# Optimization experiments

Measured on AMD Instinct MI355X. Metric: run time of the kernel, lower is better.

The kernel has to match this reference:

```python
import jax, jax.numpy as jnp
import numpy as np

B, S, CTXD, QD, ATTD = 32, 4096, 512, 512, 256

def setup_inputs() -> dict:
    key = jax.random.key(0)
    ks = jax.random.split(key, 7)
    qry = jax.random.normal(ks[0], (B, QD), dtype=jnp.float32)
    ctx = jax.random.normal(ks[1], (B, S, CTXD), dtype=jnp.float32)
    ctx_mask = jax.random.randint(ks[2], (B, S), 0, 2, dtype=jnp.int32)
    # ensure no all-zero row (would make softmax NaN)
    ctx_mask = ctx_mask.at[:, 0].set(1)
    sc = 1.0 / np.sqrt(CTXD + QD)
    W = jax.random.uniform(ks[3], (CTXD + QD, ATTD), jnp.float32, -sc, sc)
    b = jax.random.uniform(ks[4], (ATTD,), jnp.float32, -sc, sc)
    sc2 = 1.0 / np.sqrt(ATTD)
    w2 = jax.random.uniform(ks[5], (ATTD, 1), jnp.float32, -sc2, sc2)
    b2 = jax.random.uniform(ks[6], (1,), jnp.float32, -sc2, sc2)
    return {"qry": qry, "ctx": ctx, "ctx_mask": ctx_mask, "W": W, "b": b, "w2": w2, "b2": b2}

def reference(qry, ctx, ctx_mask, W, b, w2, b2):
    # cat([ctx, qry_rep]) @ W == ctx @ W_ctx + qry @ W_qry ; avoids the [B,S,ctxdim+qdim] concat
    W_ctx, W_qry = W[:CTXD], W[CTXD:]
    h = jnp.einsum('bsc,ca->bsa', ctx, W_ctx) + (qry @ W_qry)[:, None, :] + b  # [B,S,ATTD]
    y = jnp.tanh(h)
    scores = jnp.einsum('bsa,a->bs', y, w2[:, 0]) + b2[0]  # [B,S]
    scores = scores + jnp.log(ctx_mask.astype(jnp.float32))
    alphas = jax.nn.softmax(scores, axis=-1)  # [B,S]
    summary = jnp.einsum('bsc,bs->bc', ctx, alphas)  # [B,CTXD]
    return (alphas, summary, scores)
```

## Files before the change

kernel.cpp:

```cpp
#include <hip/hip_runtime.h>
#include <math.h>

#define B_ 32
#define S_ 4096
#define CTXD_ 512
#define QD_ 512
#define ATTD_ 256

#define KT 64
#define RT 64
#define NCH (S_ / RT)

#define MASKED_SCORE (-1e30f)

typedef __attribute__((ext_vector_type(8))) short bf16x8;
typedef __attribute__((ext_vector_type(4))) float f32x4;

__device__ __forceinline__ unsigned short f2bf(float f) {
    unsigned u = __float_as_uint(f);
    u += 0x7fff + ((u >> 16) & 1);
    return (unsigned short)(u >> 16);
}
__device__ __forceinline__ unsigned pk2(float lo, float hi) {
    return (unsigned)f2bf(lo) | ((unsigned)f2bf(hi) << 16);
}

__device__ __forceinline__ float fast_tanh(float x) {
    float xc = fminf(fmaxf(x, -15.f), 15.f);
    float t = __expf(2.f * xc);
    return (t - 1.f) / (t + 1.f);
}

__global__ __launch_bounds__(256) void prep_kernel(
    const float* __restrict__ W, const float* __restrict__ qry,
    const float* __restrict__ bias, unsigned short* __restrict__ Wt,
    float* __restrict__ qh) {
    __shared__ unsigned char lds[64 * 66 * 2];
    const int bid = blockIdx.x;
    const int t = threadIdx.x;
    if (bid < 32) {
        unsigned short(*tile)[66] = (unsigned short(*)[66])lds;
        const int kk = (bid >> 2) * 64;
        const int nn = (bid & 3) * 64;
        #pragma unroll
        for (int i = 0; i < 4; ++i) {
            const int r = i * 16 + (t >> 4);
            float4 v = ((const float4*)(W + (size_t)(kk + r) * ATTD_ + nn))[t & 15];
            unsigned short* tr = &tile[r][(t & 15) * 4];
            tr[0] = f2bf(v.x); tr[1] = f2bf(v.y);
            tr[2] = f2bf(v.z); tr[3] = f2bf(v.w);
        }
        __syncthreads();
        const int l8 = (t & 7) * 8;
        #pragma unroll
        for (int p = 0; p < 2; ++p) {
            const int n = p * 32 + (t >> 3);
            uint4 o;
            o.x = (unsigned)tile[l8 + 0][n] | ((unsigned)tile[l8 + 1][n] << 16);
            o.y = (unsigned)tile[l8 + 2][n] | ((unsigned)tile[l8 + 3][n] << 16);
            o.z = (unsigned)tile[l8 + 4][n] | ((unsigned)tile[l8 + 5][n] << 16);
            o.w = (unsigned)tile[l8 + 6][n] | ((unsigned)tile[l8 + 7][n] << 16);
            *(uint4*)(Wt + (size_t)(nn + n) * CTXD_ + kk + l8) = o;
        }
    } else {
        float* q = (float*)lds;
        const int b = bid - 32;
        for (int i = t; i < QD_; i += 256) q[i] = qry[b * QD_ + i];
        __syncthreads();
        float acc = bias[t];
        const float* Wq = W + (size_t)CTXD_ * ATTD_ + t;
        #pragma unroll 8
        for (int k = 0; k < QD_; ++k) acc += q[k] * Wq[(size_t)k * ATTD_];
        qh[b * ATTD_ + t] = acc;
    }
}

__global__ __launch_bounds__(256, 3) void scores_kernel(
    const float* __restrict__ ctx, const unsigned short* __restrict__ Wt,
    const float* __restrict__ qh, const float* __restrict__ w2,
    const float* __restrict__ b2, const int* __restrict__ mask,
    float* __restrict__ scores, float* __restrict__ mstat,
    float* __restrict__ lstat, float* __restrict__ part) {
    __shared__ unsigned char lds_a[RT * 144];
    __shared__ unsigned char lds_b[ATTD_ * 144];
    const int t = threadIdx.x;
    const int b = blockIdx.y;
    const int ch = blockIdx.x;
    const int s0 = ch * RT;
    const int tx = t & 63;
    const int w = t >> 6;
    const int wm = w & 1;
    const int wn = w >> 1;
    const int frow = tx & 15;
    const int fq = tx >> 4;

    f32x4 c00, c01, c02, c03, c04, c05, c06, c07;
    f32x4 c10, c11, c12, c13, c14, c15, c16, c17;
    c00 = c01 = c02 = c03 = c04 = c05 = c06 = c07 = (f32x4)0.f;
    c10 = c11 = c12 = c13 = c14 = c15 = c16 = c17 = (f32x4)0.f;

    const float* ctxb = ctx + ((size_t)b * S_ + s0) * CTXD_;
    const int arow = t >> 2;
    const int akq = t & 3;
    const int bn = t;

    const unsigned char* aBase = lds_a + (wm * 32 + frow) * 144 + fq * 16;
    const unsigned char* bBase = lds_b + (wn * 128 + frow) * 144 + fq * 16;

    const float* sA = ctxb + (size_t)arow * CTXD_ + akq * 16;
    float4 fa0 = ((const float4*)sA)[0];
    float4 fa1 = ((const float4*)sA)[1];
    float4 fa2 = ((const float4*)sA)[2];
    float4 fa3 = ((const float4*)sA)[3];
    const uint4* sB = (const uint4*)(Wt + (size_t)bn * CTXD_);
    uint4 pb0 = sB[0], pb1 = sB[1], pb2 = sB[2], pb3 = sB[3];
    uint4 pb4 = sB[4], pb5 = sB[5], pb6 = sB[6], pb7 = sB[7];

#define MM1(ni, ks, C0, C1)                                                  \
    {                                                                        \
        bf16x8 bf = *(const bf16x8*)(bBase + (ni) * (16 * 144) + (ks) * 64); \
        C0 = __builtin_amdgcn_mfma_f32_16x16x32_bf16(a0, bf, C0, 0, 0, 0);   \
        C1 = __builtin_amdgcn_mfma_f32_16x16x32_bf16(a1, bf, C1, 0, 0, 0);   \
    }
#define MMK(ks)                                                              \
    {                                                                        \
        bf16x8 a0 = *(const bf16x8*)(aBase + (ks) * 64);                     \
        bf16x8 a1 = *(const bf16x8*)(aBase + 16 * 144 + (ks) * 64);          \
        MM1(0, ks, c00, c10) MM1(1, ks, c01, c11) MM1(2, ks, c02, c12)       \
        MM1(3, ks, c03, c13) MM1(4, ks, c04, c14) MM1(5, ks, c05, c15)       \
        MM1(6, ks, c06, c16) MM1(7, ks, c07, c17)                            \
    }

    #pragma unroll 1
    for (int k0 = 0; k0 < CTXD_; k0 += KT) {
        __syncthreads();
        {
            uint4 p;
            p.x = pk2(fa0.x, fa0.y); p.y = pk2(fa0.z, fa0.w);
            p.z = pk2(fa1.x, fa1.y); p.w = pk2(fa1.z, fa1.w);
            *(uint4*)(lds_a + arow * 144 + akq * 32) = p;
            p.x = pk2(fa2.x, fa2.y); p.y = pk2(fa2.z, fa2.w);
            p.z = pk2(fa3.x, fa3.y); p.w = pk2(fa3.z, fa3.w);
            *(uint4*)(lds_a + arow * 144 + akq * 32 + 16) = p;
            uint4* bw = (uint4*)(lds_b + bn * 144);
            bw[0] = pb0; bw[1] = pb1; bw[2] = pb2; bw[3] = pb3;
            bw[4] = pb4; bw[5] = pb5; bw[6] = pb6; bw[7] = pb7;
        }
        __syncthreads();
        if (k0 + KT < CTXD_) {
            const float* sA2 = ctxb + (size_t)arow * CTXD_ + (k0 + KT) + akq * 16;
            fa0 = ((const float4*)sA2)[0];
            fa1 = ((const float4*)sA2)[1];
            fa2 = ((const float4*)sA2)[2];
            fa3 = ((const float4*)sA2)[3];
            const uint4* sB2 = (const uint4*)(Wt + (size_t)bn * CTXD_ + (k0 + KT));
            pb0 = sB2[0]; pb1 = sB2[1]; pb2 = sB2[2]; pb3 = sB2[3];
            pb4 = sB2[4]; pb5 = sB2[5]; pb6 = sB2[6]; pb7 = sB2[7];
        }
        MMK(0)
        MMK(1)
    }
#undef MMK
#undef MM1

    const float* qhb = qh + b * ATTD_ + wn * 128;
    const float* w2b = w2 + wn * 128;
    float p00 = 0.f, p01 = 0.f, p02 = 0.f, p03 = 0.f;
    float p10 = 0.f, p11 = 0.f, p12 = 0.f, p13 = 0.f;
#define EPI(ni, C0, C1)                                                      \
    {                                                                        \
        float qv = qhb[(ni) * 16 + frow];                                    \
        float wv = w2b[(ni) * 16 + frow];                                    \
        p00 += fast_tanh(C0[0] + qv) * wv;                                   \
        p01 += fast_tanh(C0[1] + qv) * wv;                                   \
        p02 += fast_tanh(C0[2] + qv) * wv;                                   \
        p03 += fast_tanh(C0[3] + qv) * wv;                                   \
        p10 += fast_tanh(C1[0] + qv) * wv;                                   \
        p11 += fast_tanh(C1[1] + qv) * wv;                                   \
        p12 += fast_tanh(C1[2] + qv) * wv;                                   \
        p13 += fast_tanh(C1[3] + qv) * wv;                                   \
    }
    EPI(0, c00, c10) EPI(1, c01, c11) EPI(2, c02, c12) EPI(3, c03, c13)
    EPI(4, c04, c14) EPI(5, c05, c15) EPI(6, c06, c16) EPI(7, c07, c17)
#undef EPI
    #pragma unroll
    for (int off = 1; off <= 8; off <<= 1) {
        p00 += __shfl_xor(p00, off, 64);
        p01 += __shfl_xor(p01, off, 64);
        p02 += __shfl_xor(p02, off, 64);
        p03 += __shfl_xor(p03, off, 64);
        p10 += __shfl_xor(p10, off, 64);
        p11 += __shfl_xor(p11, off, 64);
        p12 += __shfl_xor(p12, off, 64);
        p13 += __shfl_xor(p13, off, 64);
    }
    float* sred = (float*)lds_a;
    __syncthreads();
    if (frow == 0) {
        const int base = wn * 64 + wm * 32 + fq * 4;
        sred[base + 0] = p00; sred[base + 1] = p01;
        sred[base + 2] = p02; sred[base + 3] = p03;
        sred[base + 16 + 0] = p10; sred[base + 16 + 1] = p11;
        sred[base + 16 + 2] = p12; sred[base + 16 + 3] = p13;
    }
    __syncthreads();
    float* wl = (float*)lds_b;
    if (t < 64) {
        const int s = s0 + t;
        float sc = sred[t] + sred[64 + t] + b2[0];
        const bool msk = (mask[b * S_ + s] == 0);
        if (msk) sc = MASKED_SCORE;
        scores[b * S_ + s] = sc;
        float mloc = sc;
        #pragma unroll
        for (int off = 1; off < 64; off <<= 1)
            mloc = fmaxf(mloc, __shfl_xor(mloc, off, 64));
        const float ws = msk ? 0.f : __expf(sc - mloc);
        float lloc = ws;
        #pragma unroll
        for (int off = 1; off < 64; off <<= 1)
            lloc += __shfl_xor(lloc, off, 64);
        if (t == 0) {
            mstat[b * NCH + ch] = mloc;
            lstat[b * NCH + ch] = lloc;
        }
        wl[t] = ws;
    }
    __syncthreads();
    const int col = t & 63;
    const int q = t >> 6;
    float4 alo = make_float4(0.f, 0.f, 0.f, 0.f);
    float4 ahi = make_float4(0.f, 0.f, 0.f, 0.f);
    #pragma unroll 4
    for (int s = q; s < RT; s += 4) {
        const float al = wl[s];
        const float4* row = (const float4*)(ctxb + (size_t)s * CTXD_);
        float4 v0 = row[col];
        float4 v1 = row[col + 64];
        alo.x += v0.x * al; alo.y += v0.y * al;
        alo.z += v0.z * al; alo.w += v0.w * al;
        ahi.x += v1.x * al; ahi.y += v1.y * al;
        ahi.z += v1.z * al; ahi.w += v1.w * al;
    }
    float4* buf = (float4*)(lds_b + 1024);
    buf[q * 128 + col] = alo;
    buf[q * 128 + col + 64] = ahi;
    __syncthreads();
    if (t < 128) {
        float4 a0 = buf[t], a1 = buf[128 + t], a2 = buf[256 + t], a3 = buf[384 + t];
        float4 r;
        r.x = a0.x + a1.x + a2.x + a3.x;
        r.y = a0.y + a1.y + a2.y + a3.y;
        r.z = a0.z + a1.z + a2.z + a3.z;
        r.w = a0.w + a1.w + a2.w + a3.w;
        ((float4*)(part + ((size_t)(b * NCH + ch)) * CTXD_))[t] = r;
    }
}

__global__ __launch_bounds__(256) void combine_kernel(
    const float* __restrict__ mstat, const float* __restrict__ lstat,
    const float* __restrict__ part, const float* __restrict__ scores,
    float* __restrict__ alphas, float* __restrict__ summary) {
    const int b = blockIdx.y, seg = blockIdx.x, t = threadIdx.x;
    __shared__ float e[NCH];
    __shared__ float gstat[2];
    if (t < NCH) {
        const float mi = mstat[b * NCH + t];
        const float li = lstat[b * NCH + t];
        float m = mi;
        #pragma unroll
        for (int off = 1; off < 64; off <<= 1)
            m = fmaxf(m, __shfl_xor(m, off, 64));
        const float ei = __expf(mi - m);
        float l = ei * li;
        #pragma unroll
        for (int off = 1; off < 64; off <<= 1)
            l += __shfl_xor(l, off, 64);
        e[t] = ei;
        if (t == 0) { gstat[0] = m; gstat[1] = 1.0f / l; }
    }
    __syncthreads();
    const float m = gstat[0], il = gstat[1];
    const int c4 = t & 31;
    const int grp = t >> 5;
    float4 acc = make_float4(0.f, 0.f, 0.f, 0.f);
    for (int chv = grp; chv < NCH; chv += 8) {
        const float ei = e[chv];
        float4 v =
            ((const float4*)(part + ((size_t)(b * NCH + chv)) * CTXD_ + seg * 128))[c4];
        acc.x += ei * v.x; acc.y += ei * v.y;
        acc.z += ei * v.z; acc.w += ei * v.w;
    }
    __shared__ float4 buf[8][32];
    buf[grp][c4] = acc;
    __syncthreads();
    if (t < 32) {
        float4 r = make_float4(0.f, 0.f, 0.f, 0.f);
        #pragma unroll
        for (int g = 0; g < 8; ++g) {
            float4 v = buf[g][t];
            r.x += v.x; r.y += v.y; r.z += v.z; r.w += v.w;
        }
        r.x *= il; r.y *= il; r.z *= il; r.w *= il;
        ((float4*)(summary + (size_t)b * CTXD_ + seg * 128))[t] = r;
    }
    const int sbase = seg * 1024;
    #pragma unroll
    for (int i = 0; i < 4; ++i) {
        const int s = sbase + i * 256 + t;
        alphas[b * S_ + s] = __expf(scores[b * S_ + s] - m) * il;
    }
}

extern "C" void kernel_launch(void* const* d_in, const int* in_sizes, int n_in,
                              void* d_out, int out_size, void* d_ws,
                              size_t ws_size, hipStream_t stream) {
    const float* qry = (const float*)d_in[0];
    const float* ctx = (const float*)d_in[1];
    const int* mask = (const int*)d_in[2];
    const float* W = (const float*)d_in[3];
    const float* bias = (const float*)d_in[4];
    const float* w2 = (const float*)d_in[5];
    const float* b2 = (const float*)d_in[6];

    float* out = (float*)d_out;
    float* alphas = out;
    float* summary = out + B_ * S_;
    float* scores = out + B_ * S_ + B_ * CTXD_;

    unsigned short* Wt = (unsigned short*)d_ws;
    float* qh = (float*)((char*)d_ws + (size_t)ATTD_ * CTXD_ * 2);
    float* mstat = qh + B_ * ATTD_;
    float* lstat = mstat + B_ * NCH;
    float* part = lstat + B_ * NCH;

    prep_kernel<<<64, 256, 0, stream>>>(W, qry, bias, Wt, qh);
    scores_kernel<<<dim3(NCH, B_), 256, 0, stream>>>(ctx, Wt, qh, w2, b2, mask,
                                                     scores, mstat, lstat, part);
    combine_kernel<<<dim3(4, B_), 256, 0, stream>>>(mstat, lstat, part, scores,
                                                    alphas, summary);
}
```

Before: 449.1 us.

## Pre-swizzle W into MFMA fragment layout and feed MFMAs directly from global memory

The prep kernel now writes W_ctx in bf16, already arranged in the per-lane MFMA fragment order. The scores kernel drops LDS staging and its per-step barriers: each lane loads its ctx fragment straight from global memory, converts it to bf16 in registers, and loads B fragments from the swizzled buffer, across a fully unrolled K loop. This removes LDS traffic and synchronisation, but leaves no explicit prefetch overlap, raises register pressure (launch bounds drop from 3 to 2), and has each wave re-read W through the cache.

```diff
diff --git a/kernel.cpp b/kernel.cpp
--- a/kernel.cpp
+++ b/kernel.cpp
@@ -7,7 +7,6 @@
 #define QD_ 512
 #define ATTD_ 256
 
-#define KT 64
 #define RT 64
 #define NCH (S_ / RT)
 
@@ -24,6 +23,19 @@
 __device__ __forceinline__ unsigned pk2(float lo, float hi) {
     return (unsigned)f2bf(lo) | ((unsigned)f2bf(hi) << 16);
 }
+__device__ __forceinline__ bf16x8 cvt8(float4 lo, float4 hi) {
+    union { unsigned u[4]; bf16x8 v; } r;
+    r.u[0] = pk2(lo.x, lo.y);
+    r.u[1] = pk2(lo.z, lo.w);
+    r.u[2] = pk2(hi.x, hi.y);
+    r.u[3] = pk2(hi.z, hi.w);
+    return r.v;
+}
+__device__ __forceinline__ bf16x8 ld_bf8(const unsigned short* p) {
+    union { uint4 q; bf16x8 v; } r;
+    r.q = *(const uint4*)p;
+    return r.v;
+}
 
 __device__ __forceinline__ float fast_tanh(float x) {
     float xc = fminf(fmaxf(x, -15.f), 15.f);
@@ -33,38 +45,30 @@
 
 __global__ __launch_bounds__(256) void prep_kernel(
     const float* __restrict__ W, const float* __restrict__ qry,
-    const float* __restrict__ bias, unsigned short* __restrict__ Wt,
+    const float* __restrict__ bias, unsigned short* __restrict__ Wtf,
     float* __restrict__ qh) {
-    __shared__ unsigned char lds[64 * 66 * 2];
+    __shared__ float q[QD_];
     const int bid = blockIdx.x;
     const int t = threadIdx.x;
-    if (bid < 32) {
-        unsigned short(*tile)[66] = (unsigned short(*)[66])lds;
-        const int kk = (bid >> 2) * 64;
-        const int nn = (bid & 3) * 64;
-        #pragma unroll
-        for (int i = 0; i < 4; ++i) {
-            const int r = i * 16 + (t >> 4);
-            float4 v = ((const float4*)(W + (size_t)(kk + r) * ATTD_ + nn))[t & 15];
-            unsigned short* tr = &tile[r][(t & 15) * 4];
-            tr[0] = f2bf(v.x); tr[1] = f2bf(v.y);
-            tr[2] = f2bf(v.z); tr[3] = f2bf(v.w);
-        }
-        __syncthreads();
-        const int l8 = (t & 7) * 8;
-        #pragma unroll
-        for (int p = 0; p < 2; ++p) {
-            const int n = p * 32 + (t >> 3);
+    if (bid < 16) {
+        const int n16 = bid;
+        const int lane = t & 63;
+        const int ksl = t >> 6;
+        const int ncol = n16 * 16 + (lane & 15);
+        #pragma unroll
+        for (int r = 0; r < 4; ++r) {
+            const int ks = ksl + r * 4;
+            const int krow = ks * 32 + (lane >> 4) * 8;
+            const float* src = W + (size_t)krow * ATTD_ + ncol;
             uint4 o;
-            o.x = (unsigned)tile[l8 + 0][n] | ((unsigned)tile[l8 + 1][n] << 16);
-            o.y = (unsigned)tile[l8 + 2][n] | ((unsigned)tile[l8 + 3][n] << 16);
-            o.z = (unsigned)tile[l8 + 4][n] | ((unsigned)tile[l8 + 5][n] << 16);
-            o.w = (unsigned)tile[l8 + 6][n] | ((unsigned)tile[l8 + 7][n] << 16);
-            *(uint4*)(Wt + (size_t)(nn + n) * CTXD_ + kk + l8) = o;
+            o.x = pk2(src[0], src[ATTD_]);
+            o.y = pk2(src[2 * ATTD_], src[3 * ATTD_]);
+            o.z = pk2(src[4 * ATTD_], src[5 * ATTD_]);
+            o.w = pk2(src[6 * ATTD_], src[7 * ATTD_]);
+            *(uint4*)(Wtf + ((size_t)(n16 * 16 + ks) * 64 + lane) * 8) = o;
         }
     } else {
-        float* q = (float*)lds;
-        const int b = bid - 32;
+        const int b = bid - 16;
         for (int i = t; i < QD_; i += 256) q[i] = qry[b * QD_ + i];
         __syncthreads();
         float acc = bias[t];
@@ -75,14 +79,15 @@
     }
 }
 
-__global__ __launch_bounds__(256, 3) void scores_kernel(
-    const float* __restrict__ ctx, const unsigned short* __restrict__ Wt,
+__global__ __launch_bounds__(256, 2) void scores_kernel(
+    const float* __restrict__ ctx, const unsigned short* __restrict__ Wtf,
     const float* __restrict__ qh, const float* __restrict__ w2,
     const float* __restrict__ b2, const int* __restrict__ mask,
     float* __restrict__ scores, float* __restrict__ mstat,
     float* __restrict__ lstat, float* __restrict__ part) {
-    __shared__ unsigned char lds_a[RT * 144];
-    __shared__ unsigned char lds_b[ATTD_ * 144];
+    __shared__ float sred[128];
+    __shared__ float wl[64];
+    __shared__ float4 pbuf[512];
     const int t = threadIdx.x;
     const int b = blockIdx.y;
     const int ch = blockIdx.x;
@@ -100,66 +105,31 @@
     c10 = c11 = c12 = c13 = c14 = c15 = c16 = c17 = (f32x4)0.f;
 
     const float* ctxb = ctx + ((size_t)b * S_ + s0) * CTXD_;
-    const int arow = t >> 2;
-    const int akq = t & 3;
-    const int bn = t;
-
-    const unsigned char* aBase = lds_a + (wm * 32 + frow) * 144 + fq * 16;
-    const unsigned char* bBase = lds_b + (wn * 128 + frow) * 144 + fq * 16;
-
-    const float* sA = ctxb + (size_t)arow * CTXD_ + akq * 16;
-    float4 fa0 = ((const float4*)sA)[0];
-    float4 fa1 = ((const float4*)sA)[1];
-    float4 fa2 = ((const float4*)sA)[2];
-    float4 fa3 = ((const float4*)sA)[3];
-    const uint4* sB = (const uint4*)(Wt + (size_t)bn * CTXD_);
-    uint4 pb0 = sB[0], pb1 = sB[1], pb2 = sB[2], pb3 = sB[3];
-    uint4 pb4 = sB[4], pb5 = sB[5], pb6 = sB[6], pb7 = sB[7];
-
-#define MM1(ni, ks, C0, C1)                                                  \
+    const float* aR0 = ctxb + (size_t)(wm * 32 + frow) * CTXD_ + fq * 8;
+    const float* aR1 = aR0 + (size_t)16 * CTXD_;
+    const unsigned short* bB = Wtf + ((size_t)(wn * 8) * 16 * 64 + tx) * 8;
+
+#define MM1(ni, ks)                                                          \
     {                                                                        \
-        bf16x8 bf = *(const bf16x8*)(bBase + (ni) * (16 * 144) + (ks) * 64); \
-        C0 = __builtin_amdgcn_mfma_f32_16x16x32_bf16(a0, bf, C0, 0, 0, 0);   \
-        C1 = __builtin_amdgcn_mfma_f32_16x16x32_bf16(a1, bf, C1, 0, 0, 0);   \
+        bf16x8 bf = ld_bf8(bB + ((size_t)((ni) * 16 + (ks)) * 64) * 8);      \
+        c0##ni = __builtin_amdgcn_mfma_f32_16x16x32_bf16(a0, bf, c0##ni, 0, 0, 0); \
+        c1##ni = __builtin_amdgcn_mfma_f32_16x16x32_bf16(a1, bf, c1##ni, 0, 0, 0); \
     }
 #define MMK(ks)                                                              \
     {                                                                        \
-        bf16x8 a0 = *(const bf16x8*)(aBase + (ks) * 64);                     \
-        bf16x8 a1 = *(const bf16x8*)(aBase + 16 * 144 + (ks) * 64);          \
-        MM1(0, ks, c00, c10) MM1(1, ks, c01, c11) MM1(2, ks, c02, c12)       \
-        MM1(3, ks, c03, c13) MM1(4, ks, c04, c14) MM1(5, ks, c05, c15)       \
-        MM1(6, ks, c06, c16) MM1(7, ks, c07, c17)                            \
-    }
-
-    #pragma unroll 1
-    for (int k0 = 0; k0 < CTXD_; k0 += KT) {
-        __syncthreads();
-        {
-            uint4 p;
-            p.x = pk2(fa0.x, fa0.y); p.y = pk2(fa0.z, fa0.w);
-            p.z = pk2(fa1.x, fa1.y); p.w = pk2(fa1.z, fa1.w);
-            *(uint4*)(lds_a + arow * 144 + akq * 32) = p;
-            p.x = pk2(fa2.x, fa2.y); p.y = pk2(fa2.z, fa2.w);
-            p.z = pk2(fa3.x, fa3.y); p.w = pk2(fa3.z, fa3.w);
-            *(uint4*)(lds_a + arow * 144 + akq * 32 + 16) = p;
-            uint4* bw = (uint4*)(lds_b + bn * 144);
-            bw[0] = pb0; bw[1] = pb1; bw[2] = pb2; bw[3] = pb3;
-            bw[4] = pb4; bw[5] = pb5; bw[6] = pb6; bw[7] = pb7;
-        }
-        __syncthreads();
-        if (k0 + KT < CTXD_) {
-            const float* sA2 = ctxb + (size_t)arow * CTXD_ + (k0 + KT) + akq * 16;
-            fa0 = ((const float4*)sA2)[0];
-            fa1 = ((const float4*)sA2)[1];
-            fa2 = ((const float4*)sA2)[2];
-            fa3 = ((const float4*)sA2)[3];
-            const uint4* sB2 = (const uint4*)(Wt + (size_t)bn * CTXD_ + (k0 + KT));
-            pb0 = sB2[0]; pb1 = sB2[1]; pb2 = sB2[2]; pb3 = sB2[3];
-            pb4 = sB2[4]; pb5 = sB2[5]; pb6 = sB2[6]; pb7 = sB2[7];
-        }
-        MMK(0)
-        MMK(1)
-    }
+        float4 q0 = *(const float4*)(aR0 + (ks) * 32);                       \
+        float4 q1 = *(const float4*)(aR0 + (ks) * 32 + 4);                   \
+        float4 q2 = *(const float4*)(aR1 + (ks) * 32);                       \
+        float4 q3 = *(const float4*)(aR1 + (ks) * 32 + 4);                   \
+        bf16x8 a0 = cvt8(q0, q1);                                            \
+        bf16x8 a1 = cvt8(q2, q3);                                            \
+        MM1(0, ks) MM1(1, ks) MM1(2, ks) MM1(3, ks)                          \
+        MM1(4, ks) MM1(5, ks) MM1(6, ks) MM1(7, ks)                          \
+    }
+    MMK(0)  MMK(1)  MMK(2)  MMK(3)
+    MMK(4)  MMK(5)  MMK(6)  MMK(7)
+    MMK(8)  MMK(9)  MMK(10) MMK(11)
+    MMK(12) MMK(13) MMK(14) MMK(15)
 #undef MMK
 #undef MM1
 
@@ -167,21 +137,20 @@
     const float* w2b = w2 + wn * 128;
     float p00 = 0.f, p01 = 0.f, p02 = 0.f, p03 = 0.f;
     float p10 = 0.f, p11 = 0.f, p12 = 0.f, p13 = 0.f;
-#define EPI(ni, C0, C1)                                                      \
+#define EPI(ni)                                                              \
     {                                                                        \
         float qv = qhb[(ni) * 16 + frow];                                    \
         float wv = w2b[(ni) * 16 + frow];                                    \
-        p00 += fast_tanh(C0[0] + qv) * wv;                                   \
-        p01 += fast_tanh(C0[1] + qv) * wv;                                   \
-        p02 += fast_tanh(C0[2] + qv) * wv;                                   \
-        p03 += fast_tanh(C0[3] + qv) * wv;                                   \
-        p10 += fast_tanh(C1[0] + qv) * wv;                                   \
-        p11 += fast_tanh(C1[1] + qv) * wv;                                   \
-        p12 += fast_tanh(C1[2] + qv) * wv;                                   \
-        p13 += fast_tanh(C1[3] + qv) * wv;                                   \
-    }
-    EPI(0, c00, c10) EPI(1, c01, c11) EPI(2, c02, c12) EPI(3, c03, c13)
-    EPI(4, c04, c14) EPI(5, c05, c15) EPI(6, c06, c16) EPI(7, c07, c17)
+        p00 += fast_tanh(c0##ni[0] + qv) * wv;                               \
+        p01 += fast_tanh(c0##ni[1] + qv) * wv;                               \
+        p02 += fast_tanh(c0##ni[2] + qv) * wv;                               \
+        p03 += fast_tanh(c0##ni[3] + qv) * wv;                               \
+        p10 += fast_tanh(c1##ni[0] + qv) * wv;                               \
+        p11 += fast_tanh(c1##ni[1] + qv) * wv;                               \
+        p12 += fast_tanh(c1##ni[2] + qv) * wv;                               \
+        p13 += fast_tanh(c1##ni[3] + qv) * wv;                               \
+    }
+    EPI(0) EPI(1) EPI(2) EPI(3) EPI(4) EPI(5) EPI(6) EPI(7)
 #undef EPI
     #pragma unroll
     for (int off = 1; off <= 8; off <<= 1) {
@@ -194,8 +163,6 @@
         p12 += __shfl_xor(p12, off, 64);
         p13 += __shfl_xor(p13, off, 64);
     }
-    float* sred = (float*)lds_a;
-    __syncthreads();
     if (frow == 0) {
         const int base = wn * 64 + wm * 32 + fq * 4;
         sred[base + 0] = p00; sred[base + 1] = p01;
@@ -204,7 +171,6 @@
         sred[base + 16 + 2] = p12; sred[base + 16 + 3] = p13;
     }
     __syncthreads();
-    float* wl = (float*)lds_b;
     if (t < 64) {
         const int s = s0 + t;
         float sc = sred[t] + sred[64 + t] + b2[0];
@@ -242,12 +208,11 @@
         ahi.x += v1.x * al; ahi.y += v1.y * al;
         ahi.z += v1.z * al; ahi.w += v1.w * al;
     }
-    float4* buf = (float4*)(lds_b + 1024);
-    buf[q * 128 + col] = alo;
-    buf[q * 128 + col + 64] = ahi;
+    pbuf[q * 128 + col] = alo;
+    pbuf[q * 128 + col + 64] = ahi;
     __syncthreads();
     if (t < 128) {
-        float4 a0 = buf[t], a1 = buf[128 + t], a2 = buf[256 + t], a3 = buf[384 + t];
+        float4 a0 = pbuf[t], a1 = pbuf[128 + t], a2 = pbuf[256 + t], a3 = pbuf[384 + t];
         float4 r;
         r.x = a0.x + a1.x + a2.x + a3.x;
         r.y = a0.y + a1.y + a2.y + a3.y;
@@ -328,14 +293,14 @@
     float* summary = out + B_ * S_;
     float* scores = out + B_ * S_ + B_ * CTXD_;
 
-    unsigned short* Wt = (unsigned short*)d_ws;
+    unsigned short* Wtf = (unsigned short*)d_ws;
     float* qh = (float*)((char*)d_ws + (size_t)ATTD_ * CTXD_ * 2);
     float* mstat = qh + B_ * ATTD_;
     float* lstat = mstat + B_ * NCH;
     float* part = lstat + B_ * NCH;
 
-    prep_kernel<<<64, 256, 0, stream>>>(W, qry, bias, Wt, qh);
-    scores_kernel<<<dim3(NCH, B_), 256, 0, stream>>>(ctx, Wt, qh, w2, b2, mask,
+    prep_kernel<<<48, 256, 0, stream>>>(W, qry, bias, Wtf, qh);
+    scores_kernel<<<dim3(NCH, B_), 256, 0, stream>>>(ctx, Wtf, qh, w2, b2, mask,
                                                      scores, mstat, lstat, part);
     combine_kernel<<<dim3(4, B_), 256, 0, stream>>>(mstat, lstat, part, scores,
                                                     alphas, summary);
```

Result: slower. 560.4 us (+24.8%).

## Double-buffer LDS with fully unrolled K-loop and two-deep register prefetch

Applied to the files above, without the earlier changes.

Replaces the single-buffered K=64 loop with a fully unrolled K=32 pipeline. Two LDS buffers and two sets of prefetch registers keep two global loads in flight, and each step takes a single barrier that also waits on lgkmcnt. The goal is to overlap global loads, bf16 packing and LDS writes with the MFMA work and to halve the barriers per step. In exchange it uses more LDS (51 KB against about 46 KB before) and more live registers, which could lower occupancy under launch_bounds(256,3).

```diff
diff --git a/kernel.cpp b/kernel.cpp
--- a/kernel.cpp
+++ b/kernel.cpp
@@ -7,11 +7,16 @@
 #define QD_ 512
 #define ATTD_ 256
 
-#define KT 64
 #define RT 64
 #define NCH (S_ / RT)
 
 #define MASKED_SCORE (-1e30f)
+
+#define AOFF0 0
+#define AOFF1 5120
+#define BOFF0 10240
+#define BOFF1 30720
+#define LDS_BYTES 51200
 
 typedef __attribute__((ext_vector_type(8))) short bf16x8;
 typedef __attribute__((ext_vector_type(4))) float f32x4;
@@ -81,8 +86,7 @@
     const float* __restrict__ b2, const int* __restrict__ mask,
     float* __restrict__ scores, float* __restrict__ mstat,
     float* __restrict__ lstat, float* __restrict__ part) {
-    __shared__ unsigned char lds_a[RT * 144];
-    __shared__ unsigned char lds_b[ATTD_ * 144];
+    __shared__ __attribute__((aligned(16))) unsigned char lds[LDS_BYTES];
     const int t = threadIdx.x;
     const int b = blockIdx.y;
     const int ch = blockIdx.x;
@@ -104,84 +108,91 @@
     const int akq = t & 3;
     const int bn = t;
 
-    const unsigned char* aBase = lds_a + (wm * 32 + frow) * 144 + fq * 16;
-    const unsigned char* bBase = lds_b + (wn * 128 + frow) * 144 + fq * 16;
-
-    const float* sA = ctxb + (size_t)arow * CTXD_ + akq * 16;
-    float4 fa0 = ((const float4*)sA)[0];
-    float4 fa1 = ((const float4*)sA)[1];
-    float4 fa2 = ((const float4*)sA)[2];
-    float4 fa3 = ((const float4*)sA)[3];
-    const uint4* sB = (const uint4*)(Wt + (size_t)bn * CTXD_);
-    uint4 pb0 = sB[0], pb1 = sB[1], pb2 = sB[2], pb3 = sB[3];
-    uint4 pb4 = sB[4], pb5 = sB[5], pb6 = sB[6], pb7 = sB[7];
-
-#define MM1(ni, ks, C0, C1)                                                  \
-    {                                                                        \
-        bf16x8 bf = *(const bf16x8*)(bBase + (ni) * (16 * 144) + (ks) * 64); \
-        C0 = __builtin_amdgcn_mfma_f32_16x16x32_bf16(a0, bf, C0, 0, 0, 0);   \
-        C1 = __builtin_amdgcn_mfma_f32_16x16x32_bf16(a1, bf, C1, 0, 0, 0);   \
-    }
-#define MMK(ks)                                                              \
-    {                                                                        \
-        bf16x8 a0 = *(const bf16x8*)(aBase + (ks) * 64);                     \
-        bf16x8 a1 = *(const bf16x8*)(aBase + 16 * 144 + (ks) * 64);          \
-        MM1(0, ks, c00, c10) MM1(1, ks, c01, c11) MM1(2, ks, c02, c12)       \
-        MM1(3, ks, c03, c13) MM1(4, ks, c04, c14) MM1(5, ks, c05, c15)       \
-        MM1(6, ks, c06, c16) MM1(7, ks, c07, c17)                            \
-    }
-
-    #pragma unroll 1
-    for (int k0 = 0; k0 < CTXD_; k0 += KT) {
-        __syncthreads();
-        {
-            uint4 p;
-            p.x = pk2(fa0.x, fa0.y); p.y = pk2(fa0.z, fa0.w);
-            p.z = pk2(fa1.x, fa1.y); p.w = pk2(fa1.z, fa1.w);
-            *(uint4*)(lds_a + arow * 144 + akq * 32) = p;
-            p.x = pk2(fa2.x, fa2.y); p.y = pk2(fa2.z, fa2.w);
-            p.z = pk2(fa3.x, fa3.y); p.w = pk2(fa3.z, fa3.w);
-            *(uint4*)(lds_a + arow * 144 + akq * 32 + 16) = p;
-            uint4* bw = (uint4*)(lds_b + bn * 144);
-            bw[0] = pb0; bw[1] = pb1; bw[2] = pb2; bw[3] = pb3;
-            bw[4] = pb4; bw[5] = pb5; bw[6] = pb6; bw[7] = pb7;
-        }
-        __syncthreads();
-        if (k0 + KT < CTXD_) {
-            const float* sA2 = ctxb + (size_t)arow * CTXD_ + (k0 + KT) + akq * 16;
-            fa0 = ((const float4*)sA2)[0];
-            fa1 = ((const float4*)sA2)[1];
-            fa2 = ((const float4*)sA2)[2];
-            fa3 = ((const float4*)sA2)[3];
-            const uint4* sB2 = (const uint4*)(Wt + (size_t)bn * CTXD_ + (k0 + KT));
-            pb0 = sB2[0]; pb1 = sB2[1]; pb2 = sB2[2]; pb3 = sB2[3];
-            pb4 = sB2[4]; pb5 = sB2[5]; pb6 = sB2[6]; pb7 = sB2[7];
-        }
-        MMK(0)
-        MMK(1)
-    }
-#undef MMK
+    float4 fa0_0, fa1_0, fa0_1, fa1_1;
+    uint4 pb0_0, pb1_0, pb2_0, pb3_0;
+    uint4 pb0_1, pb1_1, pb2_1, pb3_1;
+
+#define ISSUE(S, kk)                                                         \
+    {                                                                        \
+        const float* ap = ctxb + (size_t)arow * CTXD_ + (kk) * 32 + akq * 8; \
+        fa0_##S = ((const float4*)ap)[0];                                    \
+        fa1_##S = ((const float4*)ap)[1];                                    \
+        const uint4* bp = (const uint4*)(Wt + (size_t)bn * CTXD_ + (kk) * 32); \
+        pb0_##S = bp[0]; pb1_##S = bp[1]; pb2_##S = bp[2]; pb3_##S = bp[3];  \
+    }
+#define WRITE(S, P)                                                          \
+    {                                                                        \
+        uint4 wv;                                                            \
+        wv.x = pk2(fa0_##S.x, fa0_##S.y); wv.y = pk2(fa0_##S.z, fa0_##S.w);  \
+        wv.z = pk2(fa1_##S.x, fa1_##S.y); wv.w = pk2(fa1_##S.z, fa1_##S.w);  \
+        *(uint4*)(lds + AOFF##P + arow * 80 + akq * 16) = wv;                \
+        uint4* bw = (uint4*)(lds + BOFF##P + bn * 80);                       \
+        bw[0] = pb0_##S; bw[1] = pb1_##S; bw[2] = pb2_##S; bw[3] = pb3_##S;  \
+    }
+#define MM1(ni, P)                                                           \
+    {                                                                        \
+        bf16x8 bf = *(const bf16x8*)(lds + BOFF##P +                         \
+                                     (wn * 128 + (ni) * 16 + frow) * 80 +    \
+                                     fq * 16);                               \
+        c0##ni = __builtin_amdgcn_mfma_f32_16x16x32_bf16(a0, bf, c0##ni, 0, 0, 0); \
+        c1##ni = __builtin_amdgcn_mfma_f32_16x16x32_bf16(a1, bf, c1##ni, 0, 0, 0); \
+    }
+#define COMPUTE(P)                                                           \
+    {                                                                        \
+        const unsigned char* aB = lds + AOFF##P + (wm * 32 + frow) * 80 + fq * 16; \
+        bf16x8 a0 = *(const bf16x8*)aB;                                      \
+        bf16x8 a1 = *(const bf16x8*)(aB + 16 * 80);                          \
+        MM1(0, P) MM1(1, P) MM1(2, P) MM1(3, P)                              \
+        MM1(4, P) MM1(5, P) MM1(6, P) MM1(7, P)                              \
+    }
+#define BAR                                                                  \
+    asm volatile("s_waitcnt lgkmcnt(0)" ::: "memory");                       \
+    __builtin_amdgcn_s_barrier();                                            \
+    __builtin_amdgcn_sched_barrier(0);
+
+    ISSUE(0, 0) ISSUE(1, 1)
+    WRITE(0, 0) ISSUE(0, 2)
+    BAR
+    WRITE(1, 1) ISSUE(1, 3)  COMPUTE(0) BAR
+    WRITE(0, 0) ISSUE(0, 4)  COMPUTE(1) BAR
+    WRITE(1, 1) ISSUE(1, 5)  COMPUTE(0) BAR
+    WRITE(0, 0) ISSUE(0, 6)  COMPUTE(1) BAR
+    WRITE(1, 1) ISSUE(1, 7)  COMPUTE(0) BAR
+    WRITE(0, 0) ISSUE(0, 8)  COMPUTE(1) BAR
+    WRITE(1, 1) ISSUE(1, 9)  COMPUTE(0) BAR
+    WRITE(0, 0) ISSUE(0, 10) COMPUTE(1) BAR
+    WRITE(1, 1) ISSUE(1, 11) COMPUTE(0) BAR
+    WRITE(0, 0) ISSUE(0, 12) COMPUTE(1) BAR
+    WRITE(1, 1) ISSUE(1, 13) COMPUTE(0) BAR
+    WRITE(0, 0) ISSUE(0, 14) COMPUTE(1) BAR
+    WRITE(1, 1) ISSUE(1, 15) COMPUTE(0) BAR
+    WRITE(0, 0)              COMPUTE(1) BAR
+    WRITE(1, 1)              COMPUTE(0) BAR
+    COMPUTE(1)
+#undef BAR
+#undef COMPUTE
 #undef MM1
+#undef WRITE
+#undef ISSUE
 
     const float* qhb = qh + b * ATTD_ + wn * 128;
     const float* w2b = w2 + wn * 128;
     float p00 = 0.f, p01 = 0.f, p02 = 0.f, p03 = 0.f;
     float p10 = 0.f, p11 = 0.f, p12 = 0.f, p13 = 0.f;
-#define EPI(ni, C0, C1)                                                      \
+#define EPI(ni)                                                              \
     {                                                                        \
         float qv = qhb[(ni) * 16 + frow];                                    \
         float wv = w2b[(ni) * 16 + frow];                                    \
-        p00 += fast_tanh(C0[0] + qv) * wv;                                   \
-        p01 += fast_tanh(C0[1] + qv) * wv;                                   \
-        p02 += fast_tanh(C0[2] + qv) * wv;                                   \
-        p03 += fast_tanh(C0[3] + qv) * wv;                                   \
-        p10 += fast_tanh(C1[0] + qv) * wv;                                   \
-        p11 += fast_tanh(C1[1] + qv) * wv;                                   \
-        p12 += fast_tanh(C1[2] + qv) * wv;                                   \
-        p13 += fast_tanh(C1[3] + qv) * wv;                                   \
-    }
-    EPI(0, c00, c10) EPI(1, c01, c11) EPI(2, c02, c12) EPI(3, c03, c13)
-    EPI(4, c04, c14) EPI(5, c05, c15) EPI(6, c06, c16) EPI(7, c07, c17)
+        p00 += fast_tanh(c0##ni[0] + qv) * wv;                               \
+        p01 += fast_tanh(c0##ni[1] + qv) * wv;                               \
+        p02 += fast_tanh(c0##ni[2] + qv) * wv;                               \
+        p03 += fast_tanh(c0##ni[3] + qv) * wv;                               \
+        p10 += fast_tanh(c1##ni[0] + qv) * wv;                               \
+        p11 += fast_tanh(c1##ni[1] + qv) * wv;                               \
+        p12 += fast_tanh(c1##ni[2] + qv) * wv;                               \
+        p13 += fast_tanh(c1##ni[3] + qv) * wv;                               \
+    }
+    EPI(0) EPI(1) EPI(2) EPI(3) EPI(4) EPI(5) EPI(6) EPI(7)
 #undef EPI
     #pragma unroll
     for (int off = 1; off <= 8; off <<= 1) {
@@ -194,7 +205,9 @@
         p12 += __shfl_xor(p12, off, 64);
         p13 += __shfl_xor(p13, off, 64);
     }
-    float* sred = (float*)lds_a;
+    float* sred = (float*)lds;
+    float* wl = (float*)(lds + 512);
+    float4* pbuf = (float4*)(lds + 1024);
     __syncthreads();
     if (frow == 0) {
         const int base = wn * 64 + wm * 32 + fq * 4;
@@ -204,7 +217,6 @@
         sred[base + 16 + 2] = p12; sred[base + 16 + 3] = p13;
     }
     __syncthreads();
-    float* wl = (float*)lds_b;
     if (t < 64) {
         const int s = s0 + t;
         float sc = sred[t] + sred[64 + t] + b2[0];
@@ -242,12 +254,11 @@
         ahi.x += v1.x * al; ahi.y += v1.y * al;
         ahi.z += v1.z * al; ahi.w += v1.w * al;
     }
-    float4* buf = (float4*)(lds_b + 1024);
-    buf[q * 128 + col] = alo;
-    buf[q * 128 + col + 64] = ahi;
+    pbuf[q * 128 + col] = alo;
+    pbuf[q * 128 + col + 64] = ahi;
     __syncthreads();
     if (t < 128) {
-        float4 a0 = buf[t], a1 = buf[128 + t], a2 = buf[256 + t], a3 = buf[384 + t];
+        float4 a0 = pbuf[t], a1 = pbuf[128 + t], a2 = pbuf[256 + t], a3 = pbuf[384 + t];
         float4 r;
         r.x = a0.x + a1.x + a2.x + a3.x;
         r.y = a0.y + a1.y + a2.y + a3.y;
```

After: 476.5 us. +6.1%, slower.
